# Optimization experiments

Measured on AMD Instinct MI355X. Metric: run time of the kernel, lower is better.

Reference implementation:

```python
import jax, jax.numpy as jnp
import numpy as np

N, F_IN, F_OUT, P, E = 50000, 64, 64, 8, 800000


def setup_inputs() -> dict:
    key = jax.random.key(0)
    ks = jax.random.split(key, 11)
    s = 0.05
    X = jax.random.normal(ks[0], (N, F_IN, P), jnp.float32)
    edge_index = jax.random.randint(ks[1], (2, E), 0, N)
    edge_weight = jax.random.uniform(ks[2], (E,), jnp.float32)
    # Stacked ChebConv (K=2) params for gates [i, f, c, o]
    Wx0 = jax.random.normal(ks[3], (4, F_IN, F_OUT), jnp.float32) * s
    Wx1 = jax.random.normal(ks[4], (4, F_IN, F_OUT), jnp.float32) * s
    bx = jax.random.normal(ks[5], (4, F_OUT), jnp.float32) * s
    Wh0 = jax.random.normal(ks[6], (4, F_OUT, F_OUT), jnp.float32) * s
    Wh1 = jax.random.normal(ks[7], (4, F_OUT, F_OUT), jnp.float32) * s
    bh = jax.random.normal(ks[8], (4, F_OUT), jnp.float32) * s
    wc = jax.random.normal(ks[9], (3, F_OUT), jnp.float32) * s  # peepholes for i, f, o
    bg = jax.random.normal(ks[10], (4, F_OUT), jnp.float32) * s  # gate biases i, f, c, o
    return dict(X=X, edge_index=edge_index, edge_weight=edge_weight,
                Wx0=Wx0, Wx1=Wx1, bx=bx, Wh0=Wh0, Wh1=Wh1, bh=bh, wc=wc, bg=bg)


def reference(X, edge_index, edge_weight, Wx0, Wx1, bx, Wh0, Wh1, bh, wc, bg):
    src, dst = edge_index[0], edge_index[1]
    # sym-normalized Laplacian, scaled by 2/lambda_max with lambda_max=2, minus I:
    # L_hat = -D^{-1/2} A D^{-1/2}  (diagonal cancels exactly in ChebConv.__norm__)
    deg = jax.ops.segment_sum(edge_weight, src, num_segments=N)
    dis = jnp.where(deg > 0, jax.lax.rsqrt(jnp.maximum(deg, 1e-12)), 0.0)
    wn = -dis[src] * edge_weight * dis[dst]  # [E]

    def cheb(x, W0, W1, b):
        # ChebConv K=2: T0(x)=x, T1(x)=L_hat x ; out = x@W0 + (L_hat x)@W1 + b
        tx1 = jax.ops.segment_sum(wn[:, None] * x[src], dst, num_segments=N)
        return x @ W0 + tx1 @ W1 + b

    def step(Xp):  # one GConvLSTM step from zero hidden/cell state (H=None, C=None)
        H = jnp.zeros((N, F_OUT), X.dtype)
        C = jnp.zeros((N, F_OUT), X.dtype)
        I = jax.nn.sigmoid(cheb(Xp, Wx0[0], Wx1[0], bx[0]) + cheb(H, Wh0[0], Wh1[0], bh[0]) + wc[0] * C + bg[0])
        Fg = jax.nn.sigmoid(cheb(Xp, Wx0[1], Wx1[1], bx[1]) + cheb(H, Wh0[1], Wh1[1], bh[1]) + wc[1] * C + bg[1])
        T = jnp.tanh(cheb(Xp, Wx0[2], Wx1[2], bx[2]) + cheb(H, Wh0[2], Wh1[2], bh[2]) + bg[2])
        Cn = Fg * C + I * T
        O = jax.nn.sigmoid(cheb(Xp, Wx0[3], Wx1[3], bx[3]) + cheb(H, Wh0[3], Wh1[3], bh[3]) + wc[2] * Cn + bg[3])
        return O * jnp.tanh(Cn)

    # periods are independent (fresh zero state each period) -> vmap then sum
    Hs = jax.vmap(step)(jnp.moveaxis(X, 2, 0))  # [P, N, F_OUT]
    return Hs.sum(axis=0)
```

## Files before the change

### kernel.cpp

```cpp
#include <hip/hip_runtime.h>
#include <hip/hip_fp16.h>

#define NN 50000
#define EE 800000
#define FF 64
#define PP 8
#define NPAD 50048
#define ELLW 64

typedef _Float16 half8 __attribute__((ext_vector_type(8)));
typedef float floatx4 __attribute__((ext_vector_type(4)));

static constexpr size_t al512(size_t x) { return (x + 511) & ~size_t(511); }
static constexpr size_t OFF_DEG  = 0;
static constexpr size_t OFF_CNT  = al512(OFF_DEG  + (size_t)NN*4);
static constexpr size_t OFF_DIS  = al512(OFF_CNT  + (size_t)NN*4);
static constexpr size_t OFF_ELL  = al512(OFF_DIS  + (size_t)NN*4);
static constexpr size_t OFF_BIAS = al512(OFF_ELL  + (size_t)NN*ELLW*8);
static constexpr size_t OFF_WC2  = al512(OFF_BIAS + 192*4);
static constexpr size_t OFF_WFRG = al512(OFF_WC2  + 64*4);
static constexpr size_t OFF_XB   = al512(OFF_WFRG + (size_t)24576*2);
static constexpr size_t OFF_TB   = al512(OFF_XB   + (size_t)NPAD*512*2);

__global__ void k_build(const int* __restrict__ src, const int* __restrict__ dst,
                        const float* __restrict__ ew,
                        float* __restrict__ deg, int* __restrict__ cnt,
                        int2* __restrict__ ell) {
    int e = blockIdx.x * 256 + threadIdx.x;
    if (e < EE) {
        int s = src[e], d = dst[e];
        float w = ew[e];
        atomicAdd(deg + s, w);
        int pos = atomicAdd(cnt + d, 1);
        if (pos < ELLW) {
            int2 pr; pr.x = s; pr.y = __float_as_int(w);
            ell[(size_t)d * ELLW + pos] = pr;
        }
    }
}

__global__ void k_prep(const float* __restrict__ Wx0, const float* __restrict__ Wx1,
                       const float* __restrict__ bx, const float* __restrict__ bh,
                       const float* __restrict__ wc, const float* __restrict__ bg,
                       const float* __restrict__ deg,
                       _Float16* __restrict__ Wfrag, float* __restrict__ biasv,
                       float* __restrict__ wc2, float* __restrict__ dis) {
    int t = blockIdx.x * 256 + threadIdx.x;
    const int gmap[3] = {0, 2, 3};
    if (t < NN) {
        float dg = deg[t];
        dis[t] = dg > 0.f ? rsqrtf(fmaxf(dg, 1e-12f)) : 0.f;
    }
    if (t < 24576) {
        int j8 = t & 7;
        int lane = (t >> 3) & 63;
        int rem = t >> 9;
        int ct = rem % 12;
        int ks = rem / 12;
        int k = ks * 32 + (lane >> 4) * 8 + j8;
        int gp = ct >> 2;
        int g = gmap[gp];
        int j64 = (ct & 3) * 16 + (lane & 15);
        float val = (k < 64) ? Wx0[((size_t)g * 64 + k) * 64 + j64]
                             : Wx1[((size_t)g * 64 + (k - 64)) * 64 + j64];
        Wfrag[t] = (_Float16)val;
    }
    if (t < 192) {
        int gp = t / 64, j = t % 64;
        int g = gmap[gp];
        biasv[t] = bx[g * 64 + j] + bh[g * 64 + j] + bg[g * 64 + j];
    }
    if (t < 64) wc2[t] = wc[2 * 64 + t];
}

__global__ void k_xpose(const float* __restrict__ X, _Float16* __restrict__ XB) {
    __shared__ _Float16 tile[4][512];
    int wid = threadIdx.x >> 6, lane = threadIdx.x & 63;
    int n = blockIdx.x * 4 + wid;
    if (n < NN) {
        const float4* xp = (const float4*)(X + (size_t)n * 512 + lane * 8);
        float4 a = xp[0], b = xp[1];
        float v[8] = {a.x, a.y, a.z, a.w, b.x, b.y, b.z, b.w};
#pragma unroll
        for (int p = 0; p < PP; ++p)
            tile[wid][p * 64 + lane] = (_Float16)v[p];
        half8 vv = *(const half8*)&tile[wid][lane * 8];
        *(half8*)(XB + (size_t)n * 512 + lane * 8) = vv;
    }
}

__global__ void k_spmm(const _Float16* __restrict__ XB, const int* __restrict__ cnt,
                       const float* __restrict__ dis, const int2* __restrict__ ell,
                       _Float16* __restrict__ TB) {
    int wid = threadIdx.x >> 6, lane = threadIdx.x & 63;
    int n = blockIdx.x * 4 + wid;
    if (n >= NN) return;
    float acc[8] = {0.f, 0.f, 0.f, 0.f, 0.f, 0.f, 0.f, 0.f};
    int cn = min(cnt[n], ELLW);
    float dn = dis[n];
    if (cn > 0) {
        const int2* __restrict__ row = ell + (size_t)n * ELLW;
        int2 ed = row[min(lane, cn - 1)];
        float wl = (lane < cn) ? dis[ed.x] * __int_as_float(ed.y) : 0.f;
        int wli = __float_as_int(wl);
        for (int base = 0; base < cn; base += 16) {
            half8 r[16];
            float wk[16];
#pragma unroll
            for (int u = 0; u < 16; ++u) {
                int srck = __builtin_amdgcn_readlane(ed.x, base + u);
                wk[u] = __int_as_float(__builtin_amdgcn_readlane(wli, base + u));
                r[u] = *((const half8*)(XB + (size_t)srck * 512) + lane);
            }
#pragma unroll
            for (int u = 0; u < 16; ++u) {
#pragma unroll
                for (int j = 0; j < 8; ++j) acc[j] += wk[u] * (float)r[u][j];
            }
        }
    }
    half8 st;
#pragma unroll
    for (int j = 0; j < 8; ++j) st[j] = (_Float16)(-dn * acc[j]);
    *(half8*)(TB + (size_t)n * 512 + lane * 8) = st;
}

__device__ __forceinline__ float fast_rcp(float x) { return __builtin_amdgcn_rcpf(x); }
__device__ __forceinline__ float sigmoidf_fast(float x) {
    return fast_rcp(1.f + __expf(-x));
}
__device__ __forceinline__ float tanhf_fast(float x) {
    return 1.f - 2.f * fast_rcp(1.f + __expf(2.f * x));
}

__global__ __launch_bounds__(256) void k_gemm(const _Float16* __restrict__ XB,
                                              const _Float16* __restrict__ TB,
                                              const _Float16* __restrict__ Wfrag,
                                              const float* __restrict__ biasv,
                                              const float* __restrict__ wc2,
                                              float* __restrict__ out) {
    __shared__ _Float16 Wl[24576];
    const int tid = threadIdx.x;
    const int wid = tid >> 6, lane = tid & 63;
    {
        const half8* __restrict__ Wg = (const half8*)Wfrag;
        half8* Wls = (half8*)Wl;
#pragma unroll
        for (int i = 0; i < 12; ++i) Wls[i * 256 + tid] = Wg[i * 256 + tid];
    }
    __syncthreads();
    const half8* Wl8 = (const half8*)Wl;

    const int n0 = blockIdx.x * 128 + wid * 32;
    const int jj = lane & 15, quad = lane >> 4;

    float bi[4], bc[4], bo[4], wcv[4];
#pragma unroll
    for (int c4 = 0; c4 < 4; ++c4) {
        int j = c4 * 16 + jj;
        bi[c4] = biasv[j];
        bc[c4] = biasv[64 + j];
        bo[c4] = biasv[128 + j];
        wcv[c4] = wc2[j];
    }

    const _Float16* __restrict__ x0 = XB + (size_t)(n0 + jj) * 512;
    const _Float16* __restrict__ x1 = XB + (size_t)(n0 + 16 + jj) * 512;
    const _Float16* __restrict__ t0 = TB + (size_t)(n0 + jj) * 512;
    const _Float16* __restrict__ t1 = TB + (size_t)(n0 + 16 + jj) * 512;

    floatx4 outacc[2][4];
#pragma unroll
    for (int r = 0; r < 2; ++r)
#pragma unroll
        for (int c4 = 0; c4 < 4; ++c4) outacc[r][c4] = (floatx4){0.f, 0.f, 0.f, 0.f};

#pragma unroll 1
    for (int p = 0; p < PP; ++p) {
        const int o = p * 64 + quad * 8;
        half8 a00 = *(const half8*)(x0 + o);
        half8 a01 = *(const half8*)(x0 + o + 32);
        half8 a02 = *(const half8*)(t0 + o);
        half8 a03 = *(const half8*)(t0 + o + 32);
        half8 a10 = *(const half8*)(x1 + o);
        half8 a11 = *(const half8*)(x1 + o + 32);
        half8 a12 = *(const half8*)(t1 + o);
        half8 a13 = *(const half8*)(t1 + o + 32);
#pragma unroll
        for (int c4 = 0; c4 < 4; ++c4) {
            floatx4 ai0 = {0.f,0.f,0.f,0.f}, ac0 = {0.f,0.f,0.f,0.f}, ao0 = {0.f,0.f,0.f,0.f};
            floatx4 ai1 = {0.f,0.f,0.f,0.f}, ac1 = {0.f,0.f,0.f,0.f}, ao1 = {0.f,0.f,0.f,0.f};
#pragma unroll
            for (int ks = 0; ks < 4; ++ks) {
                half8 bfi = Wl8[(ks * 12 + c4) * 64 + lane];
                half8 bfc = Wl8[(ks * 12 + 4 + c4) * 64 + lane];
                half8 bfo = Wl8[(ks * 12 + 8 + c4) * 64 + lane];
                half8 a0 = (ks == 0) ? a00 : (ks == 1) ? a01 : (ks == 2) ? a02 : a03;
                half8 a1 = (ks == 0) ? a10 : (ks == 1) ? a11 : (ks == 2) ? a12 : a13;
                ai0 = __builtin_amdgcn_mfma_f32_16x16x32_f16(a0, bfi, ai0, 0, 0, 0);
                ai1 = __builtin_amdgcn_mfma_f32_16x16x32_f16(a1, bfi, ai1, 0, 0, 0);
                ac0 = __builtin_amdgcn_mfma_f32_16x16x32_f16(a0, bfc, ac0, 0, 0, 0);
                ac1 = __builtin_amdgcn_mfma_f32_16x16x32_f16(a1, bfc, ac1, 0, 0, 0);
                ao0 = __builtin_amdgcn_mfma_f32_16x16x32_f16(a0, bfo, ao0, 0, 0, 0);
                ao1 = __builtin_amdgcn_mfma_f32_16x16x32_f16(a1, bfo, ao1, 0, 0, 0);
            }
#pragma unroll
            for (int rr = 0; rr < 4; ++rr) {
                float I0 = sigmoidf_fast(ai0[rr] + bi[c4]);
                float T0 = tanhf_fast(ac0[rr] + bc[c4]);
                float Cn0 = I0 * T0;
                float O0 = sigmoidf_fast(ao0[rr] + bo[c4] + wcv[c4] * Cn0);
                outacc[0][c4][rr] += O0 * tanhf_fast(Cn0);
                float I1 = sigmoidf_fast(ai1[rr] + bi[c4]);
                float T1 = tanhf_fast(ac1[rr] + bc[c4]);
                float Cn1 = I1 * T1;
                float O1 = sigmoidf_fast(ao1[rr] + bo[c4] + wcv[c4] * Cn1);
                outacc[1][c4][rr] += O1 * tanhf_fast(Cn1);
            }
        }
    }
#pragma unroll
    for (int r = 0; r < 2; ++r)
#pragma unroll
        for (int c4 = 0; c4 < 4; ++c4)
#pragma unroll
            for (int rr = 0; rr < 4; ++rr) {
                int n = n0 + r * 16 + quad * 4 + rr;
                if (n < NN) out[(size_t)n * 64 + c4 * 16 + jj] = outacc[r][c4][rr];
            }
}

extern "C" void kernel_launch(void* const* d_in, const int* in_sizes, int n_in,
                              void* d_out, int out_size, void* d_ws, size_t ws_size,
                              hipStream_t stream) {
    const float* X   = (const float*)d_in[0];
    const int*   ei  = (const int*)d_in[1];
    const float* ew  = (const float*)d_in[2];
    const float* Wx0 = (const float*)d_in[3];
    const float* Wx1 = (const float*)d_in[4];
    const float* bx  = (const float*)d_in[5];
    const float* bh  = (const float*)d_in[8];
    const float* wc  = (const float*)d_in[9];
    const float* bg  = (const float*)d_in[10];
    float* out = (float*)d_out;

    const int* src = ei;
    const int* dst = ei + EE;

    char* ws = (char*)d_ws;
    float* deg     = (float*)(ws + OFF_DEG);
    int*   cnt     = (int*)(ws + OFF_CNT);
    float* dis     = (float*)(ws + OFF_DIS);
    int2*  ell     = (int2*)(ws + OFF_ELL);
    float* biasv   = (float*)(ws + OFF_BIAS);
    float* wc2     = (float*)(ws + OFF_WC2);
    _Float16* Wfrag = (_Float16*)(ws + OFF_WFRG);
    _Float16* XB    = (_Float16*)(ws + OFF_XB);
    _Float16* TB    = (_Float16*)(ws + OFF_TB);

    hipMemsetAsync(ws, 0, OFF_DIS, stream);

    k_build<<<(EE + 255) / 256, 256, 0, stream>>>(src, dst, ew, deg, cnt, ell);
    k_prep<<<196, 256, 0, stream>>>(Wx0, Wx1, bx, bh, wc, bg, deg, Wfrag, biasv, wc2, dis);
    k_xpose<<<(NN + 3) / 4, 256, 0, stream>>>(X, XB);
    k_spmm<<<(NN + 3) / 4, 256, 0, stream>>>(XB, cnt, dis, ell, TB);
    k_gemm<<<(NN + 127) / 128, 256, 0, stream>>>(XB, TB, Wfrag, biasv, wc2, out);
}
```

Measured before the change: 459.0 us.

## Split SpMM feature dimension across two blocks and precompute edge weights

The SpMM kernel now launches twice as many blocks, each handling half of the 512 fp16 features per node with 8-byte loads, which raises parallelism and occupancy for the gather. A new k_wfix kernel folds dis[src] into the stored ELL edge weights once, so the SpMM no longer does a dependent dis gather per edge. In exchange, the ELL index rows are read twice, each gathered row segment is smaller, and there is an extra kernel launch.

Result: no change. 454.6 us (-1.0%).

```diff
diff --git a/kernel.cpp b/kernel.cpp
--- a/kernel.cpp
+++ b/kernel.cpp
@@ -9,6 +9,7 @@
 #define ELLW 64
 
 typedef _Float16 half8 __attribute__((ext_vector_type(8)));
+typedef _Float16 half4 __attribute__((ext_vector_type(4)));
 typedef float floatx4 __attribute__((ext_vector_type(4)));
 
 static constexpr size_t al512(size_t x) { return (x + 511) & ~size_t(511); }
@@ -73,6 +74,20 @@
     if (t < 64) wc2[t] = wc[2 * 64 + t];
 }
 
+__global__ void k_wfix(const float* __restrict__ dis, const int* __restrict__ cnt,
+                       int2* __restrict__ ell) {
+    int wid = threadIdx.x >> 6, lane = threadIdx.x & 63;
+    int n = blockIdx.x * 4 + wid;
+    if (n >= NN) return;
+    int cn = min(cnt[n], ELLW);
+    if (lane < cn) {
+        int2* p = ell + (size_t)n * ELLW + lane;
+        int2 ed = *p;
+        float w = dis[ed.x] * __int_as_float(ed.y);
+        p->y = __float_as_int(w);
+    }
+}
+
 __global__ void k_xpose(const float* __restrict__ X, _Float16* __restrict__ XB) {
     __shared__ _Float16 tile[4][512];
     int wid = threadIdx.x >> 6, lane = threadIdx.x & 63;
@@ -93,36 +108,38 @@
                        const float* __restrict__ dis, const int2* __restrict__ ell,
                        _Float16* __restrict__ TB) {
     int wid = threadIdx.x >> 6, lane = threadIdx.x & 63;
-    int n = blockIdx.x * 4 + wid;
+    int b = blockIdx.x;
+    int half = b & 1;
+    int n = (b >> 1) * 4 + wid;
     if (n >= NN) return;
-    float acc[8] = {0.f, 0.f, 0.f, 0.f, 0.f, 0.f, 0.f, 0.f};
+    float acc[4] = {0.f, 0.f, 0.f, 0.f};
     int cn = min(cnt[n], ELLW);
     float dn = dis[n];
+    const int foff = half * 256 + lane * 4;
     if (cn > 0) {
         const int2* __restrict__ row = ell + (size_t)n * ELLW;
         int2 ed = row[min(lane, cn - 1)];
-        float wl = (lane < cn) ? dis[ed.x] * __int_as_float(ed.y) : 0.f;
-        int wli = __float_as_int(wl);
+        int wli = (lane < cn) ? ed.y : 0;
         for (int base = 0; base < cn; base += 16) {
-            half8 r[16];
+            half4 r[16];
             float wk[16];
 #pragma unroll
             for (int u = 0; u < 16; ++u) {
                 int srck = __builtin_amdgcn_readlane(ed.x, base + u);
                 wk[u] = __int_as_float(__builtin_amdgcn_readlane(wli, base + u));
-                r[u] = *((const half8*)(XB + (size_t)srck * 512) + lane);
+                r[u] = *(const half4*)(XB + (size_t)srck * 512 + foff);
             }
 #pragma unroll
             for (int u = 0; u < 16; ++u) {
 #pragma unroll
-                for (int j = 0; j < 8; ++j) acc[j] += wk[u] * (float)r[u][j];
+                for (int j = 0; j < 4; ++j) acc[j] += wk[u] * (float)r[u][j];
             }
         }
     }
-    half8 st;
-#pragma unroll
-    for (int j = 0; j < 8; ++j) st[j] = (_Float16)(-dn * acc[j]);
-    *(half8*)(TB + (size_t)n * 512 + lane * 8) = st;
+    half4 st;
+#pragma unroll
+    for (int j = 0; j < 4; ++j) st[j] = (_Float16)(-dn * acc[j]);
+    *(half4*)(TB + (size_t)n * 512 + foff) = st;
 }
 
 __device__ __forceinline__ float fast_rcp(float x) { return __builtin_amdgcn_rcpf(x); }
@@ -262,7 +279,8 @@
 
     k_build<<<(EE + 255) / 256, 256, 0, stream>>>(src, dst, ew, deg, cnt, ell);
     k_prep<<<196, 256, 0, stream>>>(Wx0, Wx1, bx, bh, wc, bg, deg, Wfrag, biasv, wc2, dis);
+    k_wfix<<<(NN + 3) / 4, 256, 0, stream>>>(dis, cnt, ell);
     k_xpose<<<(NN + 3) / 4, 256, 0, stream>>>(X, XB);
-    k_spmm<<<(NN + 3) / 4, 256, 0, stream>>>(XB, cnt, dis, ell, TB);
+    k_spmm<<<2 * ((NN + 3) / 4), 256, 0, stream>>>(XB, cnt, dis, ell, TB);
     k_gemm<<<(NN + 127) / 128, 256, 0, stream>>>(XB, TB, Wfrag, biasv, wc2, out);
 }
```
